# Kernel tuning notes

Hardware: AMD Instinct MI355X
Metric: run time of the kernel (lower is better)

## Reference

```python
import jax, jax.numpy as jnp
import numpy as np

B, H, W, C = 128, 256, 1024, 1
N_HOLES = 5
PROB = 1.0
HOLE_MINW, HOLE_MAXW = W // 10, int(W / 2.5)   # 102, 409
HOLE_MINH, HOLE_MAXH = H // 10, int(H / 2.5)   # 25, 102


def setup_inputs() -> dict:
    key = jax.random.key(0)
    k0, k1, k2, k3, k4, k5 = jax.random.split(key, 6)
    x = jax.random.normal(k0, (B, H, W, C), dtype=jnp.float32)
    # hole centers: tf.random.uniform((bsz,n), 0, dim-1, int32) -> [0, dim-1)
    xs = jax.random.randint(k1, (B, N_HOLES), 0, W - 1, dtype=jnp.int32)
    ys = jax.random.randint(k2, (B, N_HOLES), 0, H - 1, dtype=jnp.int32)
    # hole sizes: raw in [0, max-min); reference adds the min offset
    xs_w_raw = jax.random.randint(k3, (B, N_HOLES), 0, HOLE_MAXW - HOLE_MINW, dtype=jnp.int32)
    ys_h_raw = jax.random.randint(k4, (B, N_HOLES), 0, HOLE_MAXH - HOLE_MINH, dtype=jnp.int32)
    # per-hole activation uniforms (hole active iff act_rand < PROB)
    act_rand = jax.random.uniform(k5, (B, N_HOLES), dtype=jnp.float32)
    return {"x": x, "xs": xs, "ys": ys, "xs_w_raw": xs_w_raw,
            "ys_h_raw": ys_h_raw, "act_rand": act_rand}


def _build_mask(xs, ys, xs_w_raw, ys_h_raw, act_rand):
    xs_w = xs_w_raw + HOLE_MINW                      # (B, N) hole widths
    ys_h = ys_h_raw + HOLE_MINH                      # (B, N) hole heights
    xs_start = jnp.clip(xs - xs_w // 2, 0, W - 2)
    xs_end   = jnp.clip(xs + xs_w // 2, 1, W - 1)
    ys_start = jnp.clip(ys - ys_h // 2, 0, H - 2)
    ys_end   = jnp.clip(ys + ys_h // 2, 1, H - 1)
    act = act_rand < PROB                            # (B, N) hole-wise activation
    idx_h = jnp.arange(H)
    idx_w = jnp.arange(W)
    mask = jnp.zeros((B, H, W), dtype=bool)
    for n in range(N_HOLES):                         # small fixed hole count
        mh = (ys_start[:, n, None] <= idx_h) & (idx_h <= ys_end[:, n, None])  # (B, H)
        mw = (xs_start[:, n, None] <= idx_w) & (idx_w <= xs_end[:, n, None])  # (B, W)
        m = mh[:, :, None] & mw[:, None, :]                                   # (B, H, W)
        mask = mask | (m & act[:, n, None, None])
    return mask


def reference(x, xs, ys, xs_w_raw, ys_h_raw, act_rand):
    mask = _build_mask(xs, ys, xs_w_raw, ys_h_raw, act_rand)   # (B, H, W) bool
    maskf = mask[..., None].astype(x.dtype)                    # (B, H, W, 1)
    fill = jnp.mean(x)  # hole_fill='min' path: hf = ones * reduce_mean(x)
    return x * (1.0 - maskf) + maskf * fill
```

## Files before the change

kernel.cpp:

```cpp
#include <hip/hip_runtime.h>


#define BB 128
#define HH 256
#define WW 1024
#define N_HOLES 5
#define HOLE_MINW (WW / 10)
#define HOLE_MINH (HH / 10)
#define N_ELEM (BB * HH * WW)
#define ROWS_PER_BLOCK 16
#define RED_BLOCKS (BB * HH / ROWS_PER_BLOCK)
#define ROW_SLICES 8
#define BATCH_ROWS 8

__global__ __launch_bounds__(256) void reduce_kernel(
    const float* __restrict__ x, float* __restrict__ partials) {
  int blk = blockIdx.x;
  int row0 = blk * ROWS_PER_BLOCK;
  int tid = threadIdx.x;

  const float4* x4 = (const float4*)x;

  float s = 0.0f;
  #pragma unroll
  for (int g = 0; g < ROWS_PER_BLOCK / BATCH_ROWS; ++g) {
    float4 v[BATCH_ROWS];
    #pragma unroll
    for (int r = 0; r < BATCH_ROWS; ++r) {
      long i = (long)(row0 + g * BATCH_ROWS + r) * (WW / 4) + tid;
      v[r] = x4[i];
    }
    #pragma unroll
    for (int r = 0; r < BATCH_ROWS; ++r) {
      s += (v[r].x + v[r].y) + (v[r].z + v[r].w);
    }
  }

  #pragma unroll
  for (int off = 32; off > 0; off >>= 1) s += __shfl_down(s, off, 64);
  __shared__ float wsum[4];
  int lane = tid & 63;
  int wave = tid >> 6;
  if (lane == 0) wsum[wave] = s;
  __syncthreads();
  if (tid == 0)
    partials[blockIdx.x] = (wsum[0] + wsum[1]) + (wsum[2] + wsum[3]);
}

__global__ __launch_bounds__(256) void fill_holes_kernel(
    const int* __restrict__ xs, const int* __restrict__ ys,
    const int* __restrict__ xs_w_raw, const int* __restrict__ ys_h_raw,
    const float* __restrict__ act_rand,
    const float* __restrict__ partials,
    float* __restrict__ out) {
  float s = 0.0f;
  for (int i = threadIdx.x; i < RED_BLOCKS; i += 256) s += partials[i];
  #pragma unroll
  for (int off = 32; off > 0; off >>= 1) s += __shfl_down(s, off, 64);
  __shared__ float wsum[4];
  __shared__ float mean_sh;
  int lane = threadIdx.x & 63;
  int wave = threadIdx.x >> 6;
  if (lane == 0) wsum[wave] = s;
  __syncthreads();
  if (threadIdx.x == 0) {
    float t = (wsum[0] + wsum[1]) + (wsum[2] + wsum[3]);
    mean_sh = t * (1.0f / (float)N_ELEM);
  }
  __syncthreads();
  float mean = mean_sh;

  int bid = blockIdx.x;
  int b = bid / (N_HOLES * ROW_SLICES);
  int rem = bid % (N_HOLES * ROW_SLICES);
  int n = rem / ROW_SLICES;
  int slice = rem % ROW_SLICES;

  int base = b * N_HOLES + n;
  if (!(act_rand[base] < 1.0f)) return;
  int cx = xs[base];
  int cy = ys[base];
  int hw = (xs_w_raw[base] + HOLE_MINW) >> 1;
  int hh = (ys_h_raw[base] + HOLE_MINH) >> 1;
  int ys_s = min(max(cy - hh, 0), HH - 2);
  int ys_e = min(max(cy + hh, 1), HH - 1);
  int xs_s = min(max(cx - hw, 0), WW - 2);
  int xs_e = min(max(cx + hw, 1), WW - 1);

  for (int h = ys_s + slice; h <= ys_e; h += ROW_SLICES) {
    long rowbase = (long)(b * HH + h) * WW;
    for (int w = xs_s + (int)threadIdx.x; w <= xs_e; w += 256) {
      out[rowbase + w] = mean;
    }
  }
}

extern "C" void kernel_launch(void* const* d_in, const int* in_sizes, int n_in,
                              void* d_out, int out_size, void* d_ws, size_t ws_size,
                              hipStream_t stream) {
  const float* x        = (const float*)d_in[0];
  const int* xs         = (const int*)d_in[1];
  const int* ys         = (const int*)d_in[2];
  const int* xs_w_raw   = (const int*)d_in[3];
  const int* ys_h_raw   = (const int*)d_in[4];
  const float* act_rand = (const float*)d_in[5];
  float* out = (float*)d_out;

  float* partials = (float*)d_ws;

  reduce_kernel<<<RED_BLOCKS, 256, 0, stream>>>(x, partials);
  hipMemcpyAsync(out, x, (size_t)N_ELEM * sizeof(float),
                 hipMemcpyDeviceToDevice, stream);
  fill_holes_kernel<<<BB * N_HOLES * ROW_SLICES, 256, 0, stream>>>(
      xs, ys, xs_w_raw, ys_h_raw, act_rand, partials, out);
}
```

Baseline: 274.1 us.

## Fuse copy and hole fill into one masked streaming apply kernel

Replaces the device-to-device memcpy plus scattered hole-fill kernel with a single kernel. It reads x with float4 loads, evaluates the five-hole mask per element in registers, and writes either x or the mean. This removes the redundant writes to hole regions and one launch. Blocks run in reverse order so the rows the reduce kernel touched last, which are most likely still in cache, are read first. Each block now recomputes the mean from the partials and does mask arithmetic per element.

```diff
diff --git a/kernel.cpp b/kernel.cpp
--- a/kernel.cpp
+++ b/kernel.cpp
@@ -10,7 +10,6 @@
 #define N_ELEM (BB * HH * WW)
 #define ROWS_PER_BLOCK 16
 #define RED_BLOCKS (BB * HH / ROWS_PER_BLOCK)
-#define ROW_SLICES 8
 #define BATCH_ROWS 8
 
 __global__ __launch_bounds__(256) void reduce_kernel(
@@ -47,50 +46,86 @@
     partials[blockIdx.x] = (wsum[0] + wsum[1]) + (wsum[2] + wsum[3]);
 }
 
-__global__ __launch_bounds__(256) void fill_holes_kernel(
+__global__ __launch_bounds__(256) void apply_kernel(
+    const float* __restrict__ x,
     const int* __restrict__ xs, const int* __restrict__ ys,
     const int* __restrict__ xs_w_raw, const int* __restrict__ ys_h_raw,
     const float* __restrict__ act_rand,
     const float* __restrict__ partials,
     float* __restrict__ out) {
-  float s = 0.0f;
-  for (int i = threadIdx.x; i < RED_BLOCKS; i += 256) s += partials[i];
-  #pragma unroll
-  for (int off = 32; off > 0; off >>= 1) s += __shfl_down(s, off, 64);
+  int tid = threadIdx.x;
+  int lane = tid & 63;
+  int wave = tid >> 6;
   __shared__ float wsum[4];
   __shared__ float mean_sh;
-  int lane = threadIdx.x & 63;
-  int wave = threadIdx.x >> 6;
-  if (lane == 0) wsum[wave] = s;
-  __syncthreads();
-  if (threadIdx.x == 0) {
-    float t = (wsum[0] + wsum[1]) + (wsum[2] + wsum[3]);
-    mean_sh = t * (1.0f / (float)N_ELEM);
+
+  {
+    float s = 0.0f;
+    for (int i = tid; i < RED_BLOCKS; i += 256) s += partials[i];
+    #pragma unroll
+    for (int off = 32; off > 0; off >>= 1) s += __shfl_down(s, off, 64);
+    if (lane == 0) wsum[wave] = s;
+    __syncthreads();
+    if (tid == 0) {
+      float t = (wsum[0] + wsum[1]) + (wsum[2] + wsum[3]);
+      mean_sh = t * (1.0f / (float)N_ELEM);
+    }
+    __syncthreads();
   }
-  __syncthreads();
   float mean = mean_sh;
 
-  int bid = blockIdx.x;
-  int b = bid / (N_HOLES * ROW_SLICES);
-  int rem = bid % (N_HOLES * ROW_SLICES);
-  int n = rem / ROW_SLICES;
-  int slice = rem % ROW_SLICES;
+  int blk = (RED_BLOCKS - 1) - blockIdx.x;
+  int b = blk >> 4;
+  int row0 = blk * ROWS_PER_BLOCK;
+  int w0 = tid * 4;
 
-  int base = b * N_HOLES + n;
-  if (!(act_rand[base] < 1.0f)) return;
-  int cx = xs[base];
-  int cy = ys[base];
-  int hw = (xs_w_raw[base] + HOLE_MINW) >> 1;
-  int hh = (ys_h_raw[base] + HOLE_MINH) >> 1;
-  int ys_s = min(max(cy - hh, 0), HH - 2);
-  int ys_e = min(max(cy + hh, 1), HH - 1);
-  int xs_s = min(max(cx - hw, 0), WW - 2);
-  int xs_e = min(max(cx + hw, 1), WW - 1);
+  int ys_s[N_HOLES], ys_e[N_HOLES], xlo[N_HOLES], xhi[N_HOLES];
+  #pragma unroll
+  for (int n = 0; n < N_HOLES; ++n) {
+    int base = b * N_HOLES + n;
+    int cx = xs[base];
+    int cy = ys[base];
+    int hw = (xs_w_raw[base] + HOLE_MINW) >> 1;
+    int hh = (ys_h_raw[base] + HOLE_MINH) >> 1;
+    bool act = act_rand[base] < 1.0f;
+    int yss = min(max(cy - hh, 0), HH - 2);
+    int yse = min(max(cy + hh, 1), HH - 1);
+    ys_s[n] = act ? yss : 1;
+    ys_e[n] = act ? yse : 0;
+    xlo[n] = min(max(cx - hw, 0), WW - 2);
+    xhi[n] = min(max(cx + hw, 1), WW - 1);
+  }
 
-  for (int h = ys_s + slice; h <= ys_e; h += ROW_SLICES) {
-    long rowbase = (long)(b * HH + h) * WW;
-    for (int w = xs_s + (int)threadIdx.x; w <= xs_e; w += 256) {
-      out[rowbase + w] = mean;
+  const float4* x4 = (const float4*)x;
+  float4* out4 = (float4*)out;
+
+  #pragma unroll
+  for (int g = 0; g < ROWS_PER_BLOCK / BATCH_ROWS; ++g) {
+    float4 v[BATCH_ROWS];
+    #pragma unroll
+    for (int r = 0; r < BATCH_ROWS; ++r) {
+      long i = (long)(row0 + g * BATCH_ROWS + r) * (WW / 4) + tid;
+      v[r] = x4[i];
+    }
+    #pragma unroll
+    for (int r = 0; r < BATCH_ROWS; ++r) {
+      int row = row0 + g * BATCH_ROWS + r;
+      int h = row & (HH - 1);
+      float rv[4] = {v[r].x, v[r].y, v[r].z, v[r].w};
+      #pragma unroll
+      for (int j = 0; j < 4; ++j) {
+        int w = w0 + j;
+        bool m = false;
+        #pragma unroll
+        for (int n = 0; n < N_HOLES; ++n)
+          m = m || ((ys_s[n] <= h) && (h <= ys_e[n]) &&
+                    (xlo[n] <= w) && (w <= xhi[n]));
+        if (m) rv[j] = mean;
+      }
+      float4 o;
+      o.x = rv[0]; o.y = rv[1]; o.z = rv[2]; o.w = rv[3];
+      long i = (long)row * (WW / 4) + tid;
+      out4[i] = o;
     }
   }
 }
@@ -109,8 +144,6 @@
   float* partials = (float*)d_ws;
 
   reduce_kernel<<<RED_BLOCKS, 256, 0, stream>>>(x, partials);
-  hipMemcpyAsync(out, x, (size_t)N_ELEM * sizeof(float),
-                 hipMemcpyDeviceToDevice, stream);
-  fill_holes_kernel<<<BB * N_HOLES * ROW_SLICES, 256, 0, stream>>>(
-      xs, ys, xs_w_raw, ys_h_raw, act_rand, partials, out);
+  apply_kernel<<<RED_BLOCKS, 256, 0, stream>>>(
+      x, xs, ys, xs_w_raw, ys_h_raw, act_rand, partials, out);
 }
```

Result: no change. 273.3 us (-0.3%).
